# Kernel tuning notes

Measured on AMD Instinct MI355X. Metric: run time of the kernel, lower is better.

## Reference

```python
import jax, jax.numpy as jnp
import numpy as np

CONF_THRESH = 0.25
IOU_THRESH = 0.45
MAX_PER_IMG = 100
K_PRE = 512          # fixed pre-NMS candidate count (padding for jit)
CLS_OFFSET = 4096.0  # class offset for non-class-agnostic NMS (torchvision batched_nms trick)


def setup_inputs() -> dict:
    key = jax.random.key(0)
    k1, k2, k3, k4 = jax.random.split(key, 4)
    B, N, C = 32, 8400, 80
    # YOLOX raw output layout: (cx, cy, w, h, obj, cls_0..cls_C-1)
    cxcy = jax.random.uniform(k1, (B, N, 2), dtype=jnp.float32) * 640.0
    wh = jax.random.uniform(k2, (B, N, 2), dtype=jnp.float32) * 128.0 + 4.0
    obj = jax.random.uniform(k3, (B, N, 1), dtype=jnp.float32)
    cls = jax.random.uniform(k4, (B, N, C), dtype=jnp.float32)
    pred = jnp.concatenate([cxcy, wh, obj, cls], axis=-1)  # [B, N, 85]
    return {"pred": pred}


def _pairwise_iou(b):
    # b: [K, 4] xyxy -> [K, K] IoU
    x1 = jnp.maximum(b[:, None, 0], b[None, :, 0])
    y1 = jnp.maximum(b[:, None, 1], b[None, :, 1])
    x2 = jnp.minimum(b[:, None, 2], b[None, :, 2])
    y2 = jnp.minimum(b[:, None, 3], b[None, :, 3])
    inter = jnp.clip(x2 - x1, 0.0) * jnp.clip(y2 - y1, 0.0)
    area = (b[:, 2] - b[:, 0]) * (b[:, 3] - b[:, 1])
    union = area[:, None] + area[None, :] - inter
    return inter / (union + 1e-9)


def _nms(boxes, valid):
    # boxes [K,4] already sorted by score desc; valid [K] bool. Greedy NMS.
    iou = _pairwise_iou(boxes)

    def body(i, keep):
        # keep[j] is False for j >= i, so this only checks earlier kept boxes
        suppressed = jnp.any(keep & (iou[i] > IOU_THRESH))
        return keep.at[i].set(valid[i] & jnp.logical_not(suppressed))

    return jax.lax.fori_loop(0, K_PRE, body, jnp.zeros(K_PRE, dtype=bool))


def reference(pred):
    # --- box decode: cxcywh -> xyxy (YOLOX postprocess box_corner) ---
    half = pred[..., 2:4] * 0.5
    boxes = jnp.concatenate([pred[..., :2] - half, pred[..., :2] + half], axis=-1)  # [B,N,4]
    obj = pred[..., 4]                 # [B,N]
    cls = pred[..., 5:]                # [B,N,C]
    class_conf = cls.max(axis=-1)      # [B,N]
    class_pred = jnp.argmax(cls, axis=-1)  # [B,N] int
    scores = obj * class_conf          # [B,N]

    # per-image adaptive conf: min(conf_thresh, best score) -> at least 1 survives
    conf = jnp.minimum(CONF_THRESH, scores.max(axis=-1, keepdims=True))  # [B,1]
    valid = scores >= conf
    masked = jnp.where(valid, scores, -jnp.inf)

    # fixed-size candidate set, sorted by score desc
    top_scores, idx = jax.lax.top_k(masked, K_PRE)  # [B,K]
    b_k = jnp.take_along_axis(boxes, idx[..., None], axis=1)       # [B,K,4]
    obj_k = jnp.take_along_axis(obj, idx, axis=1)                  # [B,K]
    cc_k = jnp.take_along_axis(class_conf, idx, axis=1)            # [B,K]
    cp_k = jnp.take_along_axis(class_pred, idx, axis=1)            # [B,K]
    valid_k = jnp.isfinite(top_scores)

    # class_agnostic=False: offset boxes by class so cross-class IoU is 0
    nms_boxes = b_k + cp_k.astype(b_k.dtype)[..., None] * CLS_OFFSET
    keep = jax.vmap(_nms)(nms_boxes, valid_k)  # [B,K] bool

    # compact kept boxes to the front (stable argsort preserves score order)
    order = jnp.argsort(jnp.where(keep, jnp.arange(K_PRE), K_PRE), axis=-1)
    sel = order[:, :MAX_PER_IMG]                                   # [B,M]
    mask = jnp.take_along_axis(keep, sel, axis=1)                  # [B,M]

    dets = jnp.concatenate(
        [b_k, obj_k[..., None], cc_k[..., None], cp_k.astype(b_k.dtype)[..., None]],
        axis=-1,
    )  # [B,K,7] = (x1,y1,x2,y2,obj,class_conf,class_pred)
    dets = jnp.take_along_axis(dets, sel[..., None], axis=1)       # [B,M,7]
    dets = dets * mask[..., None].astype(dets.dtype)
    return dets, mask
```

## Files before the change

### kernel.cpp

```cpp
#include <hip/hip_runtime.h>
#include <hip/hip_bf16.h>

#define NB 32
#define NN 8400
#define NC 80
#define KPRE 512
#define MAXOUT 100
#define NGRP 263
#define NWV 526

__global__ __launch_bounds__(128) void score_kernel(const float* __restrict__ pred,
                                                    float* __restrict__ scores,
                                                    unsigned* __restrict__ wmaxg,
                                                    float4* __restrict__ rawbox,
                                                    float4* __restrict__ minfo) {
    int b = blockIdx.y;
    int w = threadIdx.x >> 6, lane = threadIdx.x & 63;
    int g = blockIdx.x * 2 + w;
    __shared__ float4 stg4[2][340];
    const float4* p4 = (const float4*)pred;
    size_t base4 = (size_t)b * 178500 + (size_t)g * 340;
    size_t img_end4 = ((size_t)b + 1) * 178500;
    for (int k = lane; k < 340; k += 64) {
        size_t e = base4 + k;
        if (e >= img_end4) e = img_end4 - 1;
        stg4[w][k] = p4[e];
    }
    int rl = lane >> 2, q = lane & 3;
    int row = g * 16 + rl;
    const float* r = (const float*)&stg4[w][0] + rl * 85;
    float cx = r[0], cy = r[1], bw = r[2], bh = r[3], obj = r[4];
    int c0 = 5 + q * 20;
    float cc = r[c0];
    int cp = q * 20;
    for (int c = 1; c < 20; c++) {
        float v = r[c0 + c];
        if (v > cc) { cc = v; cp = q * 20 + c; }
    }
    {
        float cc1 = __shfl_xor(cc, 1, 64); int cp1 = __shfl_xor(cp, 1, 64);
        bool take = (cc1 > cc) || (cc1 == cc && cp1 < cp);
        cc = take ? cc1 : cc; cp = take ? cp1 : cp;
        float cc2 = __shfl_xor(cc, 2, 64); int cp2 = __shfl_xor(cp, 2, 64);
        take = (cc2 > cc) || (cc2 == cc && cp2 < cp);
        cc = take ? cc2 : cc; cp = take ? cp2 : cp;
    }
    float s = __fmul_rn(obj, cc);
    float hw = __fmul_rn(bw, 0.5f), hh = __fmul_rn(bh, 0.5f);
    float x1 = cx - hw, y1 = cy - hh, x2 = cx + hw, y2 = cy + hh;
    int srcl = (lane & 15) * 4;
    float v0 = __shfl(x1, srcl, 64);
    float v1 = __shfl(y1, srcl, 64);
    float v2 = __shfl(x2, srcl, 64);
    float v3 = __shfl(y2, srcl, 64);
    float v4 = __shfl(obj, srcl, 64);
    float v5 = __shfl(cc, srcl, 64);
    int   v6 = __shfl(cp, srcl, 64);
    float v7 = __shfl(s, srcl, 64);
    int wrow = g * 16 + (lane & 15);
    if (lane < 16 && wrow < NN) {
        size_t idx = (size_t)b * NN + wrow;
        scores[idx] = v7;
        rawbox[idx] = make_float4(v0, v1, v2, v3);
        minfo[idx]  = make_float4(v4, v5, (float)v6, v7);
    }
    if (row >= NN) s = 0.0f;
    unsigned bits = __float_as_uint(s);
    for (int o = 32; o > 0; o >>= 1) {
        unsigned other = (unsigned)__shfl_down((int)bits, o, 64);
        if (other > bits) bits = other;
    }
    if (lane == 0) wmaxg[b * NWV + g] = bits;
}

__device__ __forceinline__ void find_bin(const unsigned* hist, int cstart, unsigned T, int lane,
                                         int* outB, unsigned* outR) {
    unsigned running = 0;
    for (int c = cstart; c >= 0; c--) {
        unsigned v = hist[c * 64 + lane];
        unsigned s = v;
        for (int off = 1; off < 64; off <<= 1) {
            unsigned u = (unsigned)__shfl_down((int)s, off, 64);
            if (lane + off < 64) s += u;
        }
        unsigned total0 = (unsigned)__shfl((int)s, 0, 64);
        if (total0 + running >= T) {
            unsigned long long mask = __ballot(s + running >= T);
            int m = 63 - __clzll(mask);
            unsigned sm = (unsigned)__shfl((int)s, m, 64);
            unsigned vm = (unsigned)__shfl((int)v, m, 64);
            if (lane == 0) { *outB = c * 64 + m; *outR = T - (sm + running - vm); }
            return;
        }
        running += total0;
    }
    if (lane == 0) { *outB = 0; *outR = T; }
}

__global__ __launch_bounds__(1024) void select_kernel(const float* __restrict__ scores,
                                                      const unsigned* __restrict__ wmaxg,
                                                      const float4* __restrict__ rawbox,
                                                      const float4* __restrict__ minfo,
                                                      int* __restrict__ nvalid,
                                                      float4* __restrict__ boxoff,
                                                      float4* __restrict__ boxraw,
                                                      float4* __restrict__ meta) {
    int b = blockIdx.x, t = threadIdx.x;
    __shared__ unsigned histA[2048];
    __shared__ unsigned histB[2048];
    __shared__ unsigned long long list[KPRE];
    __shared__ unsigned long long sorted[KPRE];
    __shared__ unsigned long long elist64[256];
    __shared__ int S_B[2];
    __shared__ unsigned S_T[2];
    __shared__ int S_cnt, S_ecnt;
    __shared__ float S_conf;
    __shared__ unsigned S_mbits;

    if (t == 0) { S_cnt = 0; S_ecnt = 0; }
    if (t < 64) {
        unsigned m = 0;
        for (int i = t; i < NWV; i += 64) {
            unsigned v = wmaxg[b * NWV + i];
            if (v > m) m = v;
        }
        for (int off = 32; off > 0; off >>= 1) {
            unsigned o = (unsigned)__shfl_down((int)m, off, 64);
            if (o > m) m = o;
        }
        if (t == 0) { S_conf = fminf(0.25f, __uint_as_float(m)); S_mbits = m; }
    }
    for (int i = t; i < 2048; i += 1024) { histA[i] = 0; histB[i] = 0; }
    __syncthreads();
    float conf = S_conf;
    const float4* sc4 = (const float4*)(scores + (size_t)b * NN);
    unsigned ka[8];
    unsigned kb[4] = {0u, 0u, 0u, 0u};
    {
        float4 u0 = sc4[2 * t], u1 = sc4[2 * t + 1];
        ka[0] = (u0.x >= conf) ? __float_as_uint(u0.x) : 0u;
        ka[1] = (u0.y >= conf) ? __float_as_uint(u0.y) : 0u;
        ka[2] = (u0.z >= conf) ? __float_as_uint(u0.z) : 0u;
        ka[3] = (u0.w >= conf) ? __float_as_uint(u0.w) : 0u;
        ka[4] = (u1.x >= conf) ? __float_as_uint(u1.x) : 0u;
        ka[5] = (u1.y >= conf) ? __float_as_uint(u1.y) : 0u;
        ka[6] = (u1.z >= conf) ? __float_as_uint(u1.z) : 0u;
        ka[7] = (u1.w >= conf) ? __float_as_uint(u1.w) : 0u;
        if (t < 52) {
            float4 u2 = sc4[2048 + t];
            kb[0] = (u2.x >= conf) ? __float_as_uint(u2.x) : 0u;
            kb[1] = (u2.y >= conf) ? __float_as_uint(u2.y) : 0u;
            kb[2] = (u2.z >= conf) ? __float_as_uint(u2.z) : 0u;
            kb[3] = (u2.w >= conf) ? __float_as_uint(u2.w) : 0u;
        }
#pragma unroll
        for (int j = 0; j < 8; j++) atomicAdd(&histA[ka[j] >> 21], 1u);
        if (t < 52) {
#pragma unroll
            for (int j = 0; j < 4; j++) atomicAdd(&histA[kb[j] >> 21], 1u);
        }
    }
    __syncthreads();
    if (t < 64) {
        int cs = (int)(S_mbits >> 27); if (cs > 31) cs = 31;
        find_bin(histA, cs, 512u, t, &S_B[0], &S_T[0]);
    }
    __syncthreads();
    int B1 = S_B[0]; unsigned R1 = S_T[0];
#pragma unroll
    for (int j = 0; j < 8; j++) {
        unsigned k = ka[j];
        if ((int)(k >> 21) == B1) atomicAdd(&histB[(k >> 10) & 0x7FFu], 1u);
    }
    if (t < 52) {
#pragma unroll
        for (int j = 0; j < 4; j++) {
            unsigned k = kb[j];
            if ((int)(k >> 21) == B1) atomicAdd(&histB[(k >> 10) & 0x7FFu], 1u);
        }
    }
    __syncthreads();
    if (t < 64) find_bin(histB, 31, R1, t, &S_B[1], &S_T[1]);
    __syncthreads();
    unsigned P = ((unsigned)B1 << 11) | (unsigned)S_B[1];
    unsigned R2 = S_T[1];
#pragma unroll
    for (int j = 0; j < 8; j++) {
        unsigned k = ka[j];
        unsigned n = 8u * (unsigned)t + (unsigned)j;
        if ((k >> 10) > P) {
            int pos = atomicAdd(&S_cnt, 1);
            list[pos] = ((unsigned long long)k << 32) | (unsigned long long)(unsigned)(~n);
        } else if (P != 0u && (k >> 10) == P) {
            int ep = atomicAdd(&S_ecnt, 1);
            if (ep < 256) elist64[ep] = ((unsigned long long)k << 32) | (unsigned long long)(unsigned)(~n);
        }
    }
    if (t < 52) {
#pragma unroll
        for (int j = 0; j < 4; j++) {
            unsigned k = kb[j];
            unsigned n = 8192u + 4u * (unsigned)t + (unsigned)j;
            if ((k >> 10) > P) {
                int pos = atomicAdd(&S_cnt, 1);
                list[pos] = ((unsigned long long)k << 32) | (unsigned long long)(unsigned)(~n);
            } else if (P != 0u && (k >> 10) == P) {
                int ep = atomicAdd(&S_ecnt, 1);
                if (ep < 256) elist64[ep] = ((unsigned long long)k << 32) | (unsigned long long)(unsigned)(~n);
            }
        }
    }
    __syncthreads();
    int ecnt = S_ecnt; if (ecnt > 256) ecnt = 256;
    if (t < ecnt) {
        unsigned long long my = elist64[t];
        int r = 0;
        for (int j = 0; j < ecnt; j++) r += (elist64[j] > my) ? 1 : 0;
        if (r < (int)R2) {
            int pos = atomicAdd(&S_cnt, 1);
            list[pos] = my;
        }
    }
    __syncthreads();
    int nval = S_cnt;
    if (t == 0) nvalid[b] = nval;
    for (int i = nval + t; i < KPRE; i += 1024) list[i] = 0ull;
    __syncthreads();
    if (t < KPRE) {
        unsigned long long K0 = list[t];
        int r0 = 0;
        for (int j = 0; j < KPRE; j++) {
            unsigned long long L = list[j];
            r0 += (L > K0) ? 1 : 0;
        }
        if (K0 != 0ull) sorted[r0] = K0; else sorted[t] = 0ull;
    }
    __syncthreads();
    if (t < KPRE) {
        unsigned long long key = sorted[t];
        int valid = ((unsigned)(key >> 32)) != 0u;
        unsigned n = ~(unsigned)key;
        if (!valid) n = 0;
        size_t src = (size_t)b * NN + n;
        float4 rb = rawbox[src];
        float4 mi = minfo[src];
        float off = __fmul_rn(mi.z, 4096.0f);
        size_t o = (size_t)(b << 9) + t;
        boxraw[o] = rb;
        boxoff[o] = make_float4(rb.x + off, rb.y + off, rb.z + off, rb.w + off);
        meta[o] = make_float4(mi.x, mi.y, mi.z, valid ? 1.0f : 0.0f);
    }
}

__global__ __launch_bounds__(256) void iou_kernel(const float4* __restrict__ boxoff,
                                                  unsigned long long* __restrict__ ioug) {
    int b = blockIdx.y, t = threadIdx.x;
    int r = blockIdx.x * 64 + (t >> 2);
    int q = t & 3;
    __shared__ float4 sb[KPRE];
    for (int i = t; i < KPRE; i += 256) sb[i] = boxoff[(size_t)(b << 9) + i];
    __syncthreads();
    float4 bi = sb[r];
    float ai = __fmul_rn(bi.z - bi.x, bi.w - bi.y);
    unsigned long long w0 = 0ull, w1 = 0ull;
    int base = q * 128, rot = q * 33;
    for (int s = 0; s < 128; s++) {
        int jj = (s + rot) & 127;
        int jc = base + jj;
        float4 bj = sb[jc];
        float xx1 = fmaxf(bi.x, bj.x);
        float yy1 = fmaxf(bi.y, bj.y);
        float xx2 = fminf(bi.z, bj.z);
        float yy2 = fminf(bi.w, bj.w);
        float iw = fmaxf(xx2 - xx1, 0.0f);
        float ih = fmaxf(yy2 - yy1, 0.0f);
        float inter = __fmul_rn(iw, ih);
        float aj = __fmul_rn(bj.z - bj.x, bj.w - bj.y);
        float uni = (ai + aj) - inter;
        float iou = inter / (uni + 1e-9f);
        if (iou > 0.45f && jc < r) {
            if (jj < 64) w0 |= 1ull << jj;
            else         w1 |= 1ull << (jj - 64);
        }
    }
    size_t rowbase = ((size_t)(b << 9) + r) * 8 + q * 2;
    ioug[rowbase]     = w0;
    ioug[rowbase + 1] = w1;
}

__global__ __launch_bounds__(64) void scan_kernel(const unsigned long long* __restrict__ ioug,
                                                  const int* __restrict__ nvalid,
                                                  const float4* __restrict__ boxraw,
                                                  const float4* __restrict__ meta,
                                                  float* __restrict__ out) {
    int b = blockIdx.x, t = threadIdx.x;
    __shared__ unsigned long long sl[528 * 8];
    __shared__ unsigned long long skeep[8];

    const ulonglong2* src = (const ulonglong2*)(ioug + ((size_t)b << 12));
    ulonglong2* dst = (ulonglong2*)sl;
    for (int it = 0; it < 32; it++) dst[it * 64 + t] = src[it * 64 + t];
    sl[4096 + t] = 0ull;
    sl[4160 + t] = 0ull;
    __syncthreads();

    int w8 = t & 7;
    int nval = nvalid[b];
    unsigned long long keepW = 0ull;

#define STEP(ii, rwreg) { \
        bool hit = ((rwreg) & keepW) != 0ull; \
        unsigned long long bal = __ballot(hit); \
        bool kept = (bal == 0ull) && ((ii) < nval); \
        unsigned long long sb_ = (kept && (t == ((ii) >> 6))) ? (1ull << ((ii) & 63)) : 0ull; \
        keepW |= sb_; }

    unsigned long long A[8], Bf[8];
#pragma unroll
    for (int k = 0; k < 8; k++) A[k] = sl[(size_t)(0 + k) * 8 + w8];
#pragma unroll
    for (int k = 0; k < 8; k++) Bf[k] = sl[(size_t)(8 + k) * 8 + w8];
    for (int g = 0; g < 64; g += 2) {
        int base = g * 8;
#pragma unroll
        for (int k = 0; k < 8; k++) { STEP(base + k, A[k]); }
#pragma unroll
        for (int k = 0; k < 8; k++) A[k] = sl[(size_t)(base + 16 + k) * 8 + w8];
#pragma unroll
        for (int k = 0; k < 8; k++) { STEP(base + 8 + k, Bf[k]); }
#pragma unroll
        for (int k = 0; k < 8; k++) Bf[k] = sl[(size_t)(base + 24 + k) * 8 + w8];
    }
#undef STEP

    if (t < 8) skeep[t] = keepW;
    __syncthreads();

    float* dets = out + (size_t)b * (MAXOUT * 7);
    float* mask = out + (size_t)NB * MAXOUT * 7 + (size_t)b * MAXOUT;
    for (int m = t; m < MAXOUT * 7; m += 64) dets[m] = 0.0f;
    for (int m = t; m < MAXOUT; m += 64) mask[m] = 0.0f;

    for (int c = t; c < KPRE; c += 64) {
        int wq = c >> 6;
        unsigned long long kw = skeep[wq];
        int kept_c = (int)((kw >> (c & 63)) & 1ull);
        if (!kept_c) continue;
        int rank = 0;
        for (int w2 = 0; w2 < wq; w2++) rank += __popcll(skeep[w2]);
        rank += __popcll(kw & ((1ull << (c & 63)) - 1ull));
        if (rank < MAXOUT) {
            float4 rb = boxraw[(size_t)(b << 9) + c];
            float4 mt = meta[(size_t)(b << 9) + c];
            float* row = dets + rank * 7;
            row[0] = rb.x; row[1] = rb.y; row[2] = rb.z; row[3] = rb.w;
            row[4] = mt.x; row[5] = mt.y; row[6] = mt.z;
            mask[rank] = 1.0f;
        }
    }
}

extern "C" void kernel_launch(void* const* d_in, const int* in_sizes, int n_in,
                              void* d_out, int out_size, void* d_ws, size_t ws_size,
                              hipStream_t stream) {
    const float* pred = (const float*)d_in[0];
    float* out = (float*)d_out;

    char* ws = (char*)d_ws;
    unsigned* wmaxg = (unsigned*)ws;
    float* scores = (float*)(ws + 67584);
    int* nvalid = (int*)(ws + 1142784);
    float4* boxoff = (float4*)(ws + 1142912);
    float4* boxraw = (float4*)(ws + 1405056);
    float4* meta   = (float4*)(ws + 1667200);
    unsigned long long* ioug = (unsigned long long*)(ws + 1929344);
    float4* rawbox = (float4*)(ws + 2977920);
    float4* minfo  = (float4*)(ws + 7278720);

    dim3 gA(NGRP, NB);
    score_kernel<<<gA, 128, 0, stream>>>(pred, scores, wmaxg, rawbox, minfo);
    select_kernel<<<NB, 1024, 0, stream>>>(scores, wmaxg, rawbox, minfo, nvalid, boxoff, boxraw, meta);
    dim3 gI(8, NB);
    iou_kernel<<<gI, 256, 0, stream>>>(boxoff, ioug);
    scan_kernel<<<NB, 64, 0, stream>>>(ioug, nvalid, boxraw, meta, out);
}
```

Baseline: 204.3 us.

## Fuse select, IoU and NMS scan into one kernel with early exit

Folds the select, pairwise-IoU and greedy-scan kernels into a single per-image block that keeps boxes, metadata and the IoU bitmask in shared memory. It computes IoU one 64-row chunk at a time, only for lower-triangle tiles, and interleaves each chunk with the scan. The scan stops once 100 boxes are kept. This removes two launches, the global round trips for boxes and the IoU matrix, and IoU work past the point where enough boxes are kept. In exchange, only 32 blocks now do the IoU work, which lowers parallelism. The large shared-memory footprint may also limit occupancy.

```diff
diff --git a/kernel.cpp b/kernel.cpp
--- a/kernel.cpp
+++ b/kernel.cpp
@@ -1,5 +1,4 @@
 #include <hip/hip_runtime.h>
-#include <hip/hip_bf16.h>
 
 #define NB 32
 #define NN 8400
@@ -97,23 +96,26 @@
     if (lane == 0) { *outB = 0; *outR = T; }
 }
 
-__global__ __launch_bounds__(1024) void select_kernel(const float* __restrict__ scores,
+__global__ __launch_bounds__(1024) void selnms_kernel(const float* __restrict__ scores,
                                                       const unsigned* __restrict__ wmaxg,
                                                       const float4* __restrict__ rawbox,
                                                       const float4* __restrict__ minfo,
-                                                      int* __restrict__ nvalid,
-                                                      float4* __restrict__ boxoff,
-                                                      float4* __restrict__ boxraw,
-                                                      float4* __restrict__ meta) {
+                                                      float* __restrict__ out) {
     int b = blockIdx.x, t = threadIdx.x;
     __shared__ unsigned histA[2048];
     __shared__ unsigned histB[2048];
     __shared__ unsigned long long list[KPRE];
     __shared__ unsigned long long sorted[KPRE];
     __shared__ unsigned long long elist64[256];
+    __shared__ float4 sb[KPRE];
+    __shared__ float4 sraw[KPRE];
+    __shared__ float4 smeta[KPRE];
+    __shared__ float  sarea[KPRE];
+    __shared__ unsigned long long siou[KPRE * 8];
+    __shared__ unsigned long long skeep[8];
     __shared__ int S_B[2];
     __shared__ unsigned S_T[2];
-    __shared__ int S_cnt, S_ecnt;
+    __shared__ int S_cnt, S_ecnt, S_done;
     __shared__ float S_conf;
     __shared__ unsigned S_mbits;
 
@@ -131,6 +133,7 @@
         if (t == 0) { S_conf = fminf(0.25f, __uint_as_float(m)); S_mbits = m; }
     }
     for (int i = t; i < 2048; i += 1024) { histA[i] = 0; histB[i] = 0; }
+    for (int i = t; i < KPRE * 8; i += 1024) siou[i] = 0ull;
     __syncthreads();
     float conf = S_conf;
     const float4* sc4 = (const float4*)(scores + (size_t)b * NN);
@@ -223,7 +226,6 @@
     }
     __syncthreads();
     int nval = S_cnt;
-    if (t == 0) nvalid[b] = nval;
     for (int i = nval + t; i < KPRE; i += 1024) list[i] = 0ull;
     __syncthreads();
     if (t < KPRE) {
@@ -245,117 +247,89 @@
         float4 rb = rawbox[src];
         float4 mi = minfo[src];
         float off = __fmul_rn(mi.z, 4096.0f);
-        size_t o = (size_t)(b << 9) + t;
-        boxraw[o] = rb;
-        boxoff[o] = make_float4(rb.x + off, rb.y + off, rb.z + off, rb.w + off);
-        meta[o] = make_float4(mi.x, mi.y, mi.z, valid ? 1.0f : 0.0f);
-    }
-}
-
-__global__ __launch_bounds__(256) void iou_kernel(const float4* __restrict__ boxoff,
-                                                  unsigned long long* __restrict__ ioug) {
-    int b = blockIdx.y, t = threadIdx.x;
-    int r = blockIdx.x * 64 + (t >> 2);
-    int q = t & 3;
-    __shared__ float4 sb[KPRE];
-    for (int i = t; i < KPRE; i += 256) sb[i] = boxoff[(size_t)(b << 9) + i];
-    __syncthreads();
-    float4 bi = sb[r];
-    float ai = __fmul_rn(bi.z - bi.x, bi.w - bi.y);
-    unsigned long long w0 = 0ull, w1 = 0ull;
-    int base = q * 128, rot = q * 33;
-    for (int s = 0; s < 128; s++) {
-        int jj = (s + rot) & 127;
-        int jc = base + jj;
-        float4 bj = sb[jc];
-        float xx1 = fmaxf(bi.x, bj.x);
-        float yy1 = fmaxf(bi.y, bj.y);
-        float xx2 = fminf(bi.z, bj.z);
-        float yy2 = fminf(bi.w, bj.w);
-        float iw = fmaxf(xx2 - xx1, 0.0f);
-        float ih = fmaxf(yy2 - yy1, 0.0f);
-        float inter = __fmul_rn(iw, ih);
-        float aj = __fmul_rn(bj.z - bj.x, bj.w - bj.y);
-        float uni = (ai + aj) - inter;
-        float iou = inter / (uni + 1e-9f);
-        if (iou > 0.45f && jc < r) {
-            if (jj < 64) w0 |= 1ull << jj;
-            else         w1 |= 1ull << (jj - 64);
-        }
-    }
-    size_t rowbase = ((size_t)(b << 9) + r) * 8 + q * 2;
-    ioug[rowbase]     = w0;
-    ioug[rowbase + 1] = w1;
-}
-
-__global__ __launch_bounds__(64) void scan_kernel(const unsigned long long* __restrict__ ioug,
-                                                  const int* __restrict__ nvalid,
-                                                  const float4* __restrict__ boxraw,
-                                                  const float4* __restrict__ meta,
-                                                  float* __restrict__ out) {
-    int b = blockIdx.x, t = threadIdx.x;
-    __shared__ unsigned long long sl[528 * 8];
-    __shared__ unsigned long long skeep[8];
-
-    const ulonglong2* src = (const ulonglong2*)(ioug + ((size_t)b << 12));
-    ulonglong2* dst = (ulonglong2*)sl;
-    for (int it = 0; it < 32; it++) dst[it * 64 + t] = src[it * 64 + t];
-    sl[4096 + t] = 0ull;
-    sl[4160 + t] = 0ull;
-    __syncthreads();
-
-    int w8 = t & 7;
-    int nval = nvalid[b];
+        float4 bo = make_float4(rb.x + off, rb.y + off, rb.z + off, rb.w + off);
+        sraw[t] = rb;
+        sb[t] = bo;
+        smeta[t] = make_float4(mi.x, mi.y, mi.z, valid ? 1.0f : 0.0f);
+        sarea[t] = __fmul_rn(bo.z - bo.x, bo.w - bo.y);
+    }
+    __syncthreads();
+
     unsigned long long keepW = 0ull;
-
-#define STEP(ii, rwreg) { \
-        bool hit = ((rwreg) & keepW) != 0ull; \
-        unsigned long long bal = __ballot(hit); \
-        bool kept = (bal == 0ull) && ((ii) < nval); \
-        unsigned long long sb_ = (kept && (t == ((ii) >> 6))) ? (1ull << ((ii) & 63)) : 0ull; \
-        keepW |= sb_; }
-
-    unsigned long long A[8], Bf[8];
-#pragma unroll
-    for (int k = 0; k < 8; k++) A[k] = sl[(size_t)(0 + k) * 8 + w8];
-#pragma unroll
-    for (int k = 0; k < 8; k++) Bf[k] = sl[(size_t)(8 + k) * 8 + w8];
-    for (int g = 0; g < 64; g += 2) {
-        int base = g * 8;
-#pragma unroll
-        for (int k = 0; k < 8; k++) { STEP(base + k, A[k]); }
-#pragma unroll
-        for (int k = 0; k < 8; k++) A[k] = sl[(size_t)(base + 16 + k) * 8 + w8];
-#pragma unroll
-        for (int k = 0; k < 8; k++) { STEP(base + 8 + k, Bf[k]); }
-#pragma unroll
-        for (int k = 0; k < 8; k++) Bf[k] = sl[(size_t)(base + 24 + k) * 8 + w8];
-    }
-#undef STEP
-
+    int cnt = 0;
+    int lg = t >> 3, lw = t & 7;
+    int irow = t >> 4, iq = t & 15;
+
+    for (int c = 0; c < 8; c++) {
+        int row = (c << 6) + irow;
+        float4 bi = sb[row];
+        float ai = sarea[row];
+        for (int k = 0; k <= c; k++) {
+            unsigned long long wk = 0ull;
+            int j0 = (k << 6) + iq;
+#pragma unroll
+            for (int s = 0; s < 4; s++) {
+                int j = j0 + (s << 4);
+                float4 bj = sb[j];
+                float xx1 = fmaxf(bi.x, bj.x);
+                float yy1 = fmaxf(bi.y, bj.y);
+                float xx2 = fminf(bi.z, bj.z);
+                float yy2 = fminf(bi.w, bj.w);
+                float iw = fmaxf(xx2 - xx1, 0.0f);
+                float ih = fmaxf(yy2 - yy1, 0.0f);
+                float inter = __fmul_rn(iw, ih);
+                float uni = (ai + sarea[j]) - inter;
+                float iou = inter / (uni + 1e-9f);
+                if (iou > 0.45f && j < row) wk |= 1ull << (j & 63);
+            }
+            if (wk) atomicOr(&siou[(row << 3) + k], wk);
+        }
+        __syncthreads();
+        if (t < 64) {
+            unsigned long long R[8];
+#pragma unroll
+            for (int k = 0; k < 8; k++) R[k] = siou[(c << 9) + (k << 6) + t];
+#pragma unroll
+            for (int k = 0; k < 8; k++) {
+#pragma unroll
+                for (int m = 0; m < 8; m++) {
+                    int ii = (c << 6) + (k << 3) + m;
+                    bool hit = (lg == m) && ((R[k] & keepW) != 0ull);
+                    unsigned long long bal = __ballot(hit);
+                    bool kept = (bal == 0ull) && (ii < nval);
+                    if (kept) {
+                        cnt++;
+                        if (lw == c) keepW |= 1ull << ((k << 3) + m);
+                    }
+                }
+            }
+            if (t == 0) S_done = (cnt >= MAXOUT) ? 1 : 0;
+        }
+        __syncthreads();
+        if (S_done) break;
+    }
     if (t < 8) skeep[t] = keepW;
     __syncthreads();
 
     float* dets = out + (size_t)b * (MAXOUT * 7);
-    float* mask = out + (size_t)NB * MAXOUT * 7 + (size_t)b * MAXOUT;
-    for (int m = t; m < MAXOUT * 7; m += 64) dets[m] = 0.0f;
-    for (int m = t; m < MAXOUT; m += 64) mask[m] = 0.0f;
-
-    for (int c = t; c < KPRE; c += 64) {
-        int wq = c >> 6;
+    float* maskp = out + (size_t)NB * MAXOUT * 7 + (size_t)b * MAXOUT;
+    for (int m = t; m < MAXOUT * 7; m += 1024) dets[m] = 0.0f;
+    for (int m = t; m < MAXOUT; m += 1024) maskp[m] = 0.0f;
+    __syncthreads();
+    if (t < KPRE) {
+        int wq = t >> 6;
         unsigned long long kw = skeep[wq];
-        int kept_c = (int)((kw >> (c & 63)) & 1ull);
-        if (!kept_c) continue;
-        int rank = 0;
-        for (int w2 = 0; w2 < wq; w2++) rank += __popcll(skeep[w2]);
-        rank += __popcll(kw & ((1ull << (c & 63)) - 1ull));
-        if (rank < MAXOUT) {
-            float4 rb = boxraw[(size_t)(b << 9) + c];
-            float4 mt = meta[(size_t)(b << 9) + c];
-            float* row = dets + rank * 7;
-            row[0] = rb.x; row[1] = rb.y; row[2] = rb.z; row[3] = rb.w;
-            row[4] = mt.x; row[5] = mt.y; row[6] = mt.z;
-            mask[rank] = 1.0f;
+        if ((kw >> (t & 63)) & 1ull) {
+            int rank = __popcll(kw & ((1ull << (t & 63)) - 1ull));
+            for (int w2 = 0; w2 < wq; w2++) rank += __popcll(skeep[w2]);
+            if (rank < MAXOUT) {
+                float4 rb = sraw[t];
+                float4 mt = smeta[t];
+                float* rowp = dets + rank * 7;
+                rowp[0] = rb.x; rowp[1] = rb.y; rowp[2] = rb.z; rowp[3] = rb.w;
+                rowp[4] = mt.x; rowp[5] = mt.y; rowp[6] = mt.z;
+                maskp[rank] = 1.0f;
+            }
         }
     }
 }
@@ -369,18 +343,10 @@
     char* ws = (char*)d_ws;
     unsigned* wmaxg = (unsigned*)ws;
     float* scores = (float*)(ws + 67584);
-    int* nvalid = (int*)(ws + 1142784);
-    float4* boxoff = (float4*)(ws + 1142912);
-    float4* boxraw = (float4*)(ws + 1405056);
-    float4* meta   = (float4*)(ws + 1667200);
-    unsigned long long* ioug = (unsigned long long*)(ws + 1929344);
-    float4* rawbox = (float4*)(ws + 2977920);
-    float4* minfo  = (float4*)(ws + 7278720);
+    float4* rawbox = (float4*)(ws + 1142784);
+    float4* minfo  = (float4*)(ws + 5443584);
 
     dim3 gA(NGRP, NB);
     score_kernel<<<gA, 128, 0, stream>>>(pred, scores, wmaxg, rawbox, minfo);
-    select_kernel<<<NB, 1024, 0, stream>>>(scores, wmaxg, rawbox, minfo, nvalid, boxoff, boxraw, meta);
-    dim3 gI(8, NB);
-    iou_kernel<<<gI, 256, 0, stream>>>(boxoff, ioug);
-    scan_kernel<<<NB, 64, 0, stream>>>(ioug, nvalid, boxraw, meta, out);
+    selnms_kernel<<<NB, 1024, 0, stream>>>(scores, wmaxg, rawbox, minfo, out);
 }
```

Result: faster. 170.1 us (-16.8%).
